# Kernel optimization log

Measured on AMD Instinct MI355X. Metric: run time of the kernel, lower is better.

The kernel has to match this reference:

```python
import jax, jax.numpy as jnp
import numpy as np

N, E, D, B = 40000, 100000, 64, 256

def setup_inputs() -> dict:
    key = jax.random.key(0)
    ks = jax.random.split(key, 32)
    p = lambda k, shp: jax.random.normal(k, shp, dtype=jnp.float32) * 0.1
    inp = {
        'n_feat': jax.random.normal(ks[0], (N, 23), dtype=jnp.float32),
        'e_feat': jax.random.normal(ks[1], (E, 19), dtype=jnp.float32),
        'src': jax.random.randint(ks[2], (E,), 0, N, dtype=jnp.int32),
        'dst': jax.random.randint(ks[3], (E,), 0, N, dtype=jnp.int32),
        'node_graph': jnp.sort(jax.random.randint(ks[4], (N,), 0, B, dtype=jnp.int32)),
        'batch_size': B,
        'lin0_w': p(ks[5], (D, 23)), 'lin0_b': p(ks[6], (D,)),
        'en_w1': p(ks[7], (128, 19)), 'en_b1': p(ks[8], (128,)),
        'en_w2': p(ks[9], (D * D, 128)), 'en_b2': p(ks[10], (D * D,)),
        'conv_b': p(ks[11], (D,)),
        'gru_wih': p(ks[12], (3 * D, D)), 'gru_whh': p(ks[13], (3 * D, D)),
        'gru_bih': p(ks[14], (3 * D,)), 'gru_bhh': p(ks[15], (3 * D,)),
        'ls_wih0': p(ks[16], (4 * D, 2 * D)), 'ls_wih12': p(ks[17], (2, 4 * D, D)),
        'ls_whh': p(ks[18], (3, 4 * D, D)),
        'ls_bih': p(ks[19], (3, 4 * D)), 'ls_bhh': p(ks[20], (3, 4 * D)),
        'lin3_w': p(ks[21], (2 * D, 2 * D)), 'lin3_b': p(ks[22], (2 * D,)),
        'pred_w': p(ks[23], (1, 2 * D)), 'pred_b': p(ks[24], (1,)),
    }
    return inp


def _gru_step(x, h, wih, whh, bih, bhh):
    gi = x @ wih.T + bih   # (N, 3D)
    gh = h @ whh.T + bhh
    i_r, i_z, i_n = jnp.split(gi, 3, axis=-1)
    h_r, h_z, h_n = jnp.split(gh, 3, axis=-1)
    r = jax.nn.sigmoid(i_r + h_r)
    z = jax.nn.sigmoid(i_z + h_z)
    n = jnp.tanh(i_n + r * h_n)
    return (1.0 - z) * n + z * h


def _lstm_cell(x, h, c, wih, whh, bih, bhh):
    g = x @ wih.T + bih + h @ whh.T + bhh  # (B, 4D)
    i, f, gg, o = jnp.split(g, 4, axis=-1)
    c2 = jax.nn.sigmoid(f) * c + jax.nn.sigmoid(i) * jnp.tanh(gg)
    h2 = jax.nn.sigmoid(o) * jnp.tanh(c2)
    return h2, c2


def reference(n_feat, e_feat, src, dst, node_graph, batch_size,
              lin0_w, lin0_b, en_w1, en_b1, en_w2, en_b2, conv_b,
              gru_wih, gru_whh, gru_bih, gru_bhh,
              ls_wih0, ls_wih12, ls_whh, ls_bih, ls_bhh,
              lin3_w, lin3_b, pred_w, pred_b):
    d = lin0_b.shape[0]
    n_nodes = n_feat.shape[0]
    # input projection
    out = n_feat @ lin0_w.T + lin0_b                       # (N, D)
    h = out                                                # GRU hidden (1 layer)
    # edge network (same every step) -> per-edge weight matrices
    ew = jax.nn.relu(e_feat @ en_w1.T + en_b1) @ en_w2.T + en_b2
    ew = ew.reshape(-1, d, d)                              # (E, D, D)
    for _ in range(6):
        msg = jnp.einsum('ed,edf->ef', out[src], ew)       # gather + per-edge GEMM
        m = jax.ops.segment_sum(msg, dst, num_segments=n_nodes) + conv_b
        h = _gru_step(m, h, gru_wih, gru_whh, gru_bih, gru_bhh)
        out = h
    # Set2Set pooling
    hs = [jnp.zeros((batch_size, d), jnp.float32) for _ in range(3)]
    cs = [jnp.zeros((batch_size, d), jnp.float32) for _ in range(3)]
    q_star = jnp.zeros((batch_size, 2 * d), jnp.float32)
    for _ in range(6):
        x = q_star
        for l in range(3):
            wih = ls_wih0 if l == 0 else ls_wih12[l - 1]
            hs[l], cs[l] = _lstm_cell(x, hs[l], cs[l], wih, ls_whh[l], ls_bih[l], ls_bhh[l])
            x = hs[l]
        q = x                                              # (B, D)
        e = jnp.sum(out * q[node_graph], axis=-1)          # (N,)
        emax = jax.ops.segment_max(e, node_graph, num_segments=batch_size)
        ee = jnp.exp(e - emax[node_graph])
        esum = jax.ops.segment_sum(ee, node_graph, num_segments=batch_size)
        alpha = (ee / esum[node_graph])[:, None]
        readout = jax.ops.segment_sum(out * alpha, node_graph, num_segments=batch_size)
        q_star = jnp.concatenate([q, readout], axis=-1)
    y = jax.nn.relu(q_star @ lin3_w.T + lin3_b)
    predict = y @ pred_w.T + pred_b
    return h[None], predict
```

## Files before the change

kernel.cpp:

```cpp
#include <hip/hip_runtime.h>

typedef unsigned short u16;
typedef unsigned int u32;
typedef _Float16 f16;
typedef __attribute__((ext_vector_type(8))) _Float16 f16x8;
typedef __attribute__((ext_vector_type(4))) _Float16 f16x4;
typedef __attribute__((ext_vector_type(4))) float f32x4;

#define NN 40000
#define EE 100000
#define DD 64
#define BB 256
#define XTS 136
#define EPB 128

__device__ inline float sigmoidf_(float x){
    return 1.f / (1.f + __expf(-x));
}
__device__ inline float tanhf_(float x){
    x = fmaxf(fminf(x, 15.f), -15.f);
    float e = __expf(2.f * x);
    return (e - 1.f) / (e + 1.f);
}

typedef __attribute__((address_space(3))) unsigned int lds_u32;
typedef __attribute__((address_space(1))) const unsigned int g_u32;
__device__ inline void gload_lds16(const void* g, void* l){
    __builtin_amdgcn_global_load_lds((g_u32*)g, (lds_u32*)l, 16, 0, 0);
}

__global__ __launch_bounds__(256) void prep_kernel(
    const float* __restrict__ en_w2, f16* __restrict__ w2h,
    const float* __restrict__ gru_wih, const float* __restrict__ gru_whh,
    f16* __restrict__ wf16h, f16* __restrict__ wf16l,
    const float* __restrict__ ls_wih0, const float* __restrict__ ls_wih12,
    const float* __restrict__ ls_whh, float* __restrict__ lsT,
    const float* __restrict__ lin3_w, float* __restrict__ lin3T,
    const float* __restrict__ gru_bih, const float* __restrict__ conv_b,
    float* __restrict__ effb,
    const int* __restrict__ node_graph, int* __restrict__ offs)
{
    int i = blockIdx.x * 256 + threadIdx.x;
    if (i < 524288){
        w2h[i] = (f16)en_w2[i];
        return;
    }
    i -= 524288;
    if (i < 49152){
        int sel = i / 12288;
        int r = i % 12288;
        int gg = sel >> 1, islo = sel & 1;
        float v = (gg ? gru_whh : gru_wih)[r];
        f16 hi = (f16)v;
        if (islo) wf16l[gg * 12288 + r] = (f16)(v - (float)hi);
        else      wf16h[gg * 12288 + r] = hi;
        return;
    }
    i -= 49152;
    if (i < 114688){
        float v;
        if (i < 32768){
            int d = i >> 8, g = i & 255;
            v = ls_wih0[g * 128 + d];
        } else if (i < 65536){
            int j = i - 32768;
            int l = j >> 14, r = j & 16383;
            int d = r >> 8, g = r & 255;
            v = ls_wih12[l * 16384 + g * 64 + d];
        } else {
            int j = i - 65536;
            int l = j >> 14, r = j & 16383;
            int d = r >> 8, g = r & 255;
            v = ls_whh[l * 16384 + g * 64 + d];
        }
        lsT[i] = v;
        return;
    }
    i -= 114688;
    if (i < 16384){
        int ii = i >> 7, jj = i & 127;
        lin3T[i] = lin3_w[jj * 128 + ii];
        return;
    }
    i -= 16384;
    if (i < 192){
        float b = gru_bih[i];
        #pragma unroll
        for (int d = 0; d < 64; d++) b += gru_wih[i * 64 + d] * conv_b[d];
        effb[i] = b;
        return;
    }
    i -= 192;
    if (i <= 256){
        int lo = 0, hi = NN;
        while (lo < hi){
            int mid = (lo + hi) >> 1;
            if (node_graph[mid] < i) lo = mid + 1; else hi = mid;
        }
        offs[i] = lo;
        return;
    }
}

__global__ __launch_bounds__(256) void lin0_kernel(
    const float* __restrict__ nf, const float* __restrict__ w,
    const float* __restrict__ b, float* __restrict__ out)
{
    int tid = blockIdx.x * 256 + threadIdx.x;
    int n = tid >> 6, d = tid & 63;
    if (n >= NN) return;
    float acc = b[d];
    const float* nr = nf + (size_t)n * 23;
    const float* wr = w + d * 23;
    #pragma unroll
    for (int j = 0; j < 23; j++) acc = fmaf(nr[j], wr[j], acc);
    out[(size_t)n * 64 + d] = acc;
}

__global__ __launch_bounds__(256) void edge_hidden_kernel(
    const float* __restrict__ ef, const float* __restrict__ w1,
    const float* __restrict__ b1, f16* __restrict__ hidh)
{
    int tid = blockIdx.x * 256 + threadIdx.x;
    int e = tid >> 7, k = tid & 127;
    if (e >= EE) return;
    float acc = b1[k];
    const float* er = ef + (size_t)e * 19;
    const float* wr = w1 + k * 19;
    #pragma unroll
    for (int j = 0; j < 19; j++) acc = fmaf(er[j], wr[j], acc);
    acc = fmaxf(acc, 0.f);
    hidh[(size_t)e * 128 + k] = (f16)acc;
}

__global__ __launch_bounds__(512) void msg_fused_kernel(
    const float* __restrict__ h, const f16* __restrict__ hidh,
    const f16* __restrict__ w2h, const float* __restrict__ b2,
    const int* __restrict__ src, const int* __restrict__ dst,
    float* __restrict__ m)
{
    __shared__ f16 s_xT[64 * XTS];
    __shared__ f16 s_b2f[4096];
    __shared__ int s_dst[EPB];
    __shared__ f16x8 s_t0[1024], s_t1[1024], s_t2[1024];

    const int t = threadIdx.x;
    const int base = blockIdx.x * EPB;
    const int lane = t & 63;
    const int wid = t >> 6;

    int goff[2], lbase[2];
    #pragma unroll
    for (int cc = 0; cc < 2; cc++){
        int s = cc * 512 + wid * 64 + lane;
        int kh = s >> 9;
        int c2 = s & 511;
        int col = c2 >> 3;
        int jj = (c2 & 7) ^ (col & 7);
        goff[cc] = col * 128 + kh * 64 + jj * 8;
        lbase[cc] = cc * 512 + wid * 64;
    }

#define STG_ISSUE(DN, BUF)                                                   \
    {                                                                        \
        const f16* gsrc = w2h + (size_t)(DN) * 8192;                         \
        gload_lds16(gsrc + goff[0], (BUF) + lbase[0]);                       \
        gload_lds16(gsrc + goff[1], (BUF) + lbase[1]);                       \
    }

    f16x8* pb0 = s_t0;
    f16x8* pb1 = s_t1;
    f16x8* pb2 = s_t2;
    STG_ISSUE(0, pb0);
    STG_ISSUE(1, pb1);

    for (int i = t; i < EPB * 64; i += 512){
        int el = i >> 6, f = i & 63;
        int e = base + el;
        float v = 0.f;
        if (e < EE) v = h[(size_t)src[e] * 64 + f];
        s_xT[f * XTS + el] = (f16)v;
    }
    for (int i = t; i < 4096; i += 512) s_b2f[i] = (f16)b2[i];
    if (t < EPB){
        int e = base + t;
        s_dst[t] = (e < EE) ? dst[e] : -1;
    }

    const int eg = wid >> 1;
    const int fp = wid & 1;
    const int r16 = lane & 15;
    const int kg = lane >> 4;
    const int we = eg * 32;
    const int sw = r16 & 7;

    f16x8 ah[2][4];
    #pragma unroll
    for (int mt = 0; mt < 2; mt++){
        int e = base + we + mt * 16 + r16;
        #pragma unroll
        for (int ks = 0; ks < 4; ks++){
            if (e < EE){
                ah[mt][ks] = *(const f16x8*)(hidh + (size_t)e * 128 + ks * 32 + kg * 8);
            } else {
                f16x8 z = {0,0,0,0,0,0,0,0};
                ah[mt][ks] = z;
            }
        }
    }

    f32x4 msg[2][2];
    #pragma unroll
    for (int a = 0; a < 2; a++)
        #pragma unroll
        for (int b = 0; b < 2; b++){
            f32x4 z = {0.f, 0.f, 0.f, 0.f};
            msg[a][b] = z;
        }

    int rslot[2][4];
    #pragma unroll
    for (int ftl = 0; ftl < 2; ftl++){
        int col = fp * 32 + ftl * 16 + r16;
        #pragma unroll
        for (int ks = 0; ks < 4; ks++){
            int j2 = (ks & 1) * 4 + kg;
            rslot[ftl][ks] = (ks >> 1) * 512 + col * 8 + (j2 ^ sw);
        }
    }

    __syncthreads();

    for (int d = 0; d < 64; d++){
        if (d + 2 < 64) STG_ISSUE(d + 2, pb2);
        f32x4 xv[2];
        #pragma unroll
        for (int mt = 0; mt < 2; mt++){
            f16x4 xh = *(const f16x4*)&s_xT[d * XTS + we + mt * 16 + kg * 4];
            #pragma unroll
            for (int r = 0; r < 4; r++) xv[mt][r] = (float)xh[r];
        }
        __builtin_amdgcn_s_setprio(1);
        #pragma unroll
        for (int ftl = 0; ftl < 2; ftl++){
            f16x8 bf0 = pb0[rslot[ftl][0]];
            f16x8 bf1 = pb0[rslot[ftl][1]];
            f16x8 bf2 = pb0[rslot[ftl][2]];
            f16x8 bf3 = pb0[rslot[ftl][3]];
            float b2v = (float)s_b2f[d * 64 + fp * 32 + ftl * 16 + r16];
            #pragma unroll
            for (int mt = 0; mt < 2; mt++){
                f32x4 acc = {b2v, b2v, b2v, b2v};
                acc = __builtin_amdgcn_mfma_f32_16x16x32_f16(ah[mt][0], bf0, acc, 0, 0, 0);
                acc = __builtin_amdgcn_mfma_f32_16x16x32_f16(ah[mt][1], bf1, acc, 0, 0, 0);
                acc = __builtin_amdgcn_mfma_f32_16x16x32_f16(ah[mt][2], bf2, acc, 0, 0, 0);
                acc = __builtin_amdgcn_mfma_f32_16x16x32_f16(ah[mt][3], bf3, acc, 0, 0, 0);
                msg[mt][ftl] = xv[mt] * acc + msg[mt][ftl];
            }
        }
        __builtin_amdgcn_s_setprio(0);
        if (d < 63){
            if (d <= 61) asm volatile("s_waitcnt vmcnt(2)" ::: "memory");
            else         asm volatile("s_waitcnt vmcnt(0)" ::: "memory");
            __builtin_amdgcn_s_barrier();
        }
        f16x8* tmp = pb0; pb0 = pb1; pb1 = pb2; pb2 = tmp;
    }
#undef STG_ISSUE

    #pragma unroll
    for (int mt = 0; mt < 2; mt++){
        #pragma unroll
        for (int r = 0; r < 4; r++){
            int el = we + mt * 16 + kg * 4 + r;
            int dt = s_dst[el];
            if (dt >= 0){
                #pragma unroll
                for (int ftl = 0; ftl < 2; ftl++)
                    atomicAdd(&m[(size_t)dt * 64 + fp * 32 + ftl * 16 + r16],
                              msg[mt][ftl][r]);
            }
        }
    }
}

__global__ __launch_bounds__(256) void gru_mfma_kernel(
    float* __restrict__ m, float* __restrict__ h,
    const f16* __restrict__ wf16h, const f16* __restrict__ wf16l,
    const float* __restrict__ effb, const float* __restrict__ bhh)
{
    __shared__ float s_g[2][32][194];
    const int t = threadIdx.x;
    const int base = blockIdx.x * 32;
    const int lane = t & 63;
    const int wid = t >> 6;
    const int rt = wid & 1;
    const int gg = wid >> 1;
    const int r16 = lane & 15;
    const int kg = lane >> 4;

    const float* __restrict__ X = gg ? h : m;
    int n = base + rt * 16 + r16;

    f16x8 ah[2], al[2];
    #pragma unroll
    for (int ks = 0; ks < 2; ks++){
        const float* xp = X + (size_t)n * 64 + ks * 32 + kg * 8;
        f32x4 v0 = *(const f32x4*)(xp);
        f32x4 v1 = *(const f32x4*)(xp + 4);
        #pragma unroll
        for (int j = 0; j < 4; j++){
            f16 hi0 = (f16)v0[j], hi1 = (f16)v1[j];
            ah[ks][j] = hi0;     ah[ks][4 + j] = hi1;
            al[ks][j] = (f16)(v0[j] - (float)hi0);
            al[ks][4 + j] = (f16)(v1[j] - (float)hi1);
        }
    }

    const f16* __restrict__ wh = wf16h + gg * 12288;
    const f16* __restrict__ wl = wf16l + gg * 12288;
    #pragma unroll
    for (int ct = 0; ct < 12; ct++){
        int g = ct * 16 + r16;
        f16x8 bh0 = *(const f16x8*)(wh + g * 64 + kg * 8);
        f16x8 bh1 = *(const f16x8*)(wh + g * 64 + 32 + kg * 8);
        f16x8 bl0 = *(const f16x8*)(wl + g * 64 + kg * 8);
        f16x8 bl1 = *(const f16x8*)(wl + g * 64 + 32 + kg * 8);
        f32x4 acc = {0.f, 0.f, 0.f, 0.f};
        acc = __builtin_amdgcn_mfma_f32_16x16x32_f16(ah[0], bh0, acc, 0, 0, 0);
        acc = __builtin_amdgcn_mfma_f32_16x16x32_f16(ah[1], bh1, acc, 0, 0, 0);
        acc = __builtin_amdgcn_mfma_f32_16x16x32_f16(ah[0], bl0, acc, 0, 0, 0);
        acc = __builtin_amdgcn_mfma_f32_16x16x32_f16(ah[1], bl1, acc, 0, 0, 0);
        acc = __builtin_amdgcn_mfma_f32_16x16x32_f16(al[0], bh0, acc, 0, 0, 0);
        acc = __builtin_amdgcn_mfma_f32_16x16x32_f16(al[1], bh1, acc, 0, 0, 0);
        #pragma unroll
        for (int r = 0; r < 4; r++)
            s_g[gg][rt * 16 + kg * 4 + r][ct * 16 + r16] = acc[r];
    }
    __syncthreads();

    int node = t >> 3;
    int f0 = (t & 7) * 8;
    int n2 = base + node;
    #pragma unroll
    for (int j = 0; j < 8; j++){
        int f = f0 + j;
        float gir = s_g[0][node][f]       + effb[f];
        float giz = s_g[0][node][64 + f]  + effb[64 + f];
        float gin = s_g[0][node][128 + f] + effb[128 + f];
        float ghr = s_g[1][node][f]       + bhh[f];
        float ghz = s_g[1][node][64 + f]  + bhh[64 + f];
        float ghn = s_g[1][node][128 + f] + bhh[128 + f];
        float r = sigmoidf_(gir + ghr);
        float z = sigmoidf_(giz + ghz);
        float nv = tanhf_(gin + r * ghn);
        size_t hb = (size_t)n2 * 64 + f;
        float hv = h[hb];
        h[hb] = (1.f - z) * nv + z * hv;
        m[hb] = 0.f;
    }
}

__global__ __launch_bounds__(256) void set2set_kernel(
    const float* __restrict__ out, const int* __restrict__ offs,
    const float* __restrict__ lsT, const float* __restrict__ ls_bih,
    const float* __restrict__ ls_bhh, const float* __restrict__ lin3T,
    const float* __restrict__ lin3_b, const float* __restrict__ pred_w,
    const float* __restrict__ pred_b, float* __restrict__ e_ws,
    float* __restrict__ pred_out)
{
    int g = blockIdx.x;
    int t = threadIdx.x;
    int ln = t >> 6, d = t & 63;
    __shared__ float s_qstar[128], s_h[3][64], s_c[3][64], s_g[256];
    __shared__ float s_r[4][64], s_red[4], s_wsum[4], s_y[128];
    if (t < 128) s_qstar[t] = 0.f;
    if (t < 192){ s_h[t / 64][t % 64] = 0.f; s_c[t / 64][t % 64] = 0.f; }
    int ns = offs[g], ne = offs[g + 1];
    __syncthreads();

#define LSTM_GATE(L)                                                         \
    __syncthreads();                                                         \
    s_g[t] = acc;                                                            \
    __syncthreads();                                                         \
    if (t < 64){                                                             \
        float iv = s_g[t], fv = s_g[64 + t], gv = s_g[128 + t], ov = s_g[192 + t]; \
        float c2 = sigmoidf_(fv) * s_c[L][t] + sigmoidf_(iv) * tanhf_(gv);   \
        float h2 = sigmoidf_(ov) * tanhf_(c2);                               \
        s_c[L][t] = c2; s_h[L][t] = h2;                                      \
    }                                                                        \
    __syncthreads();

    for (int it = 0; it < 6; it++){
        {
            float acc = ls_bih[t] + ls_bhh[t];
            const float* wx = lsT;
            #pragma unroll 32
            for (int j = 0; j < 128; j++) acc = fmaf(s_qstar[j], wx[j * 256 + t], acc);
            const float* wh = lsT + 65536;
            #pragma unroll 32
            for (int j = 0; j < 64; j++) acc = fmaf(s_h[0][j], wh[j * 256 + t], acc);
            LSTM_GATE(0)
        }
        {
            float acc = ls_bih[256 + t] + ls_bhh[256 + t];
            const float* wx = lsT + 32768;
            #pragma unroll 32
            for (int j = 0; j < 64; j++) acc = fmaf(s_h[0][j], wx[j * 256 + t], acc);
            const float* wh = lsT + 65536 + 16384;
            #pragma unroll 32
            for (int j = 0; j < 64; j++) acc = fmaf(s_h[1][j], wh[j * 256 + t], acc);
            LSTM_GATE(1)
        }
        {
            float acc = ls_bih[512 + t] + ls_bhh[512 + t];
            const float* wx = lsT + 32768 + 16384;
            #pragma unroll 32
            for (int j = 0; j < 64; j++) acc = fmaf(s_h[1][j], wx[j * 256 + t], acc);
            const float* wh = lsT + 65536 + 2 * 16384;
            #pragma unroll 32
            for (int j = 0; j < 64; j++) acc = fmaf(s_h[2][j], wh[j * 256 + t], acc);
            LSTM_GATE(2)
        }
        float wmax = -3.4e38f;
        #pragma unroll 2
        for (int n = ns + ln; n < ne; n += 4){
            float p = out[(size_t)n * 64 + d] * s_h[2][d];
            #pragma unroll
            for (int o = 1; o < 64; o <<= 1) p += __shfl_xor(p, o);
            if (d == 0) e_ws[n] = p;
            wmax = fmaxf(wmax, p);
        }
        if (d == 0) s_red[ln] = wmax;
        __syncthreads();
        float gmax = fmaxf(fmaxf(s_red[0], s_red[1]), fmaxf(s_red[2], s_red[3]));
        float wsum = 0.f, racc = 0.f;
        #pragma unroll 2
        for (int n = ns + ln; n < ne; n += 4){
            float w = __expf(e_ws[n] - gmax);
            wsum += w;
            racc = fmaf(w, out[(size_t)n * 64 + d], racc);
        }
        s_r[ln][d] = racc;
        if (d == 0) s_wsum[ln] = wsum;
        __syncthreads();
        if (t < 64){
            float gsum = s_wsum[0] + s_wsum[1] + s_wsum[2] + s_wsum[3];
            float ro = s_r[0][t] + s_r[1][t] + s_r[2][t] + s_r[3][t];
            ro = (gsum > 0.f) ? ro / gsum : 0.f;
            s_qstar[t] = s_h[2][t];
            s_qstar[64 + t] = ro;
        }
        __syncthreads();
    }
#undef LSTM_GATE
    if (t < 128){
        float acc = lin3_b[t];
        #pragma unroll 32
        for (int i = 0; i < 128; i++) acc = fmaf(s_qstar[i], lin3T[i * 128 + t], acc);
        s_y[t] = fmaxf(acc, 0.f);
    }
    __syncthreads();
    if (t < 64){
        float p = s_y[t] * pred_w[t] + s_y[64 + t] * pred_w[64 + t];
        #pragma unroll
        for (int o = 1; o < 64; o <<= 1) p += __shfl_xor(p, o);
        if (t == 0) pred_out[g] = p + pred_b[0];
    }
}

extern "C" void kernel_launch(void* const* d_in, const int* in_sizes, int n_in,
                              void* d_out, int out_size, void* d_ws, size_t ws_size,
                              hipStream_t stream)
{
    (void)in_sizes; (void)n_in; (void)out_size; (void)ws_size;
    const float* n_feat  = (const float*)d_in[0];
    const float* e_feat  = (const float*)d_in[1];
    const int*   src     = (const int*)d_in[2];
    const int*   dst     = (const int*)d_in[3];
    const int*   node_graph = (const int*)d_in[4];
    const float* lin0_w  = (const float*)d_in[6];
    const float* lin0_b  = (const float*)d_in[7];
    const float* en_w1   = (const float*)d_in[8];
    const float* en_b1   = (const float*)d_in[9];
    const float* en_w2   = (const float*)d_in[10];
    const float* en_b2   = (const float*)d_in[11];
    const float* conv_b  = (const float*)d_in[12];
    const float* gru_wih = (const float*)d_in[13];
    const float* gru_whh = (const float*)d_in[14];
    const float* gru_bih = (const float*)d_in[15];
    const float* gru_bhh = (const float*)d_in[16];
    const float* ls_wih0 = (const float*)d_in[17];
    const float* ls_wih12= (const float*)d_in[18];
    const float* ls_whh  = (const float*)d_in[19];
    const float* ls_bih  = (const float*)d_in[20];
    const float* ls_bhh  = (const float*)d_in[21];
    const float* lin3_w  = (const float*)d_in[22];
    const float* lin3_b  = (const float*)d_in[23];
    const float* pred_w  = (const float*)d_in[24];
    const float* pred_b  = (const float*)d_in[25];

    float* h = (float*)d_out;
    float* pred_out = (float*)d_out + (size_t)NN * 64;

    char* ws = (char*)d_ws;
    f16*   hidh  = (f16*)(ws + 0);
    float* m     = (float*)(ws + 25600000);
    f16*   w2h   = (f16*)(ws + 35840000);
    f16*   wf16h = (f16*)(ws + 36888576);
    f16*   wf16l = (f16*)(ws + 36937728);
    float* lsT   = (float*)(ws + 36986880);
    float* lin3T = (float*)(ws + 37445632);
    float* effb  = (float*)(ws + 37511168);
    float* e_ws  = (float*)(ws + 37511936);
    int*   offs  = (int*)(ws + 37671936);

    prep_kernel<<<2754, 256, 0, stream>>>(en_w2, w2h, gru_wih, gru_whh,
                                          wf16h, wf16l,
                                          ls_wih0, ls_wih12, ls_whh, lsT,
                                          lin3_w, lin3T, gru_bih, conv_b, effb,
                                          node_graph, offs);
    lin0_kernel<<<(NN * 64) / 256, 256, 0, stream>>>(n_feat, lin0_w, lin0_b, h);
    edge_hidden_kernel<<<(EE * 128) / 256, 256, 0, stream>>>(e_feat, en_w1, en_b1, hidh);
    hipMemsetAsync(m, 0, (size_t)NN * 64 * sizeof(float), stream);

    for (int step = 0; step < 6; step++){
        msg_fused_kernel<<<(EE + EPB - 1) / EPB, 512, 0, stream>>>(h, hidh, w2h,
                                                                   en_b2, src, dst, m);
        gru_mfma_kernel<<<NN / 32, 256, 0, stream>>>(m, h, wf16h, wf16l, effb, gru_bhh);
    }

    set2set_kernel<<<BB, 256, 0, stream>>>(h, offs, lsT, ls_bih, ls_bhh,
                                           lin3T, lin3_b, pred_w, pred_b,
                                           e_ws, pred_out);
}
```

Baseline: 1.269 ms.

## Use single-pass online softmax with vectorized loads in set2set attention

Replaces the two-pass attention in set2set (score pass writing scores to a workspace, then a max-normalised weighted sum) with a single-pass online softmax. Each 16-thread group handles one node per iteration using float4 loads, keeps a running max, sum and readout, and the 16 partial states are merged at the end. This avoids reading node features twice and the global score scratch buffer, at the cost of extra exp calls per node for rescaling. The set2set kernel is a small part of total time next to the message-passing loop.

Measured after the change: 1.180 ms, median of 2. 1.08x faster.

```diff
diff --git a/kernel.cpp b/kernel.cpp
--- a/kernel.cpp
+++ b/kernel.cpp
@@ -366,17 +366,18 @@
     const float* __restrict__ lsT, const float* __restrict__ ls_bih,
     const float* __restrict__ ls_bhh, const float* __restrict__ lin3T,
     const float* __restrict__ lin3_b, const float* __restrict__ pred_w,
-    const float* __restrict__ pred_b, float* __restrict__ e_ws,
-    float* __restrict__ pred_out)
+    const float* __restrict__ pred_b, float* __restrict__ pred_out)
 {
     int g = blockIdx.x;
     int t = threadIdx.x;
-    int ln = t >> 6, d = t & 63;
-    __shared__ float s_qstar[128], s_h[3][64], s_c[3][64], s_g[256];
-    __shared__ float s_r[4][64], s_red[4], s_wsum[4], s_y[128];
+    __shared__ float s_qstar[128], s_h[3][64], s_c[3][64], s_g[256], s_y[128];
+    __shared__ float s_gm[16], s_gw[16];
+    __shared__ float s_gr[16][68];
     if (t < 128) s_qstar[t] = 0.f;
     if (t < 192){ s_h[t / 64][t % 64] = 0.f; s_c[t / 64][t % 64] = 0.f; }
     int ns = offs[g], ne = offs[g + 1];
+    const int lg = t >> 4;
+    const int li = t & 15;
     __syncthreads();
 
 #define LSTM_GATE(L)                                                         \
@@ -422,31 +423,37 @@
             for (int j = 0; j < 64; j++) acc = fmaf(s_h[2][j], wh[j * 256 + t], acc);
             LSTM_GATE(2)
         }
-        float wmax = -3.4e38f;
-        #pragma unroll 2
-        for (int n = ns + ln; n < ne; n += 4){
-            float p = out[(size_t)n * 64 + d] * s_h[2][d];
-            #pragma unroll
-            for (int o = 1; o < 64; o <<= 1) p += __shfl_xor(p, o);
-            if (d == 0) e_ws[n] = p;
-            wmax = fmaxf(wmax, p);
-        }
-        if (d == 0) s_red[ln] = wmax;
-        __syncthreads();
-        float gmax = fmaxf(fmaxf(s_red[0], s_red[1]), fmaxf(s_red[2], s_red[3]));
-        float wsum = 0.f, racc = 0.f;
-        #pragma unroll 2
-        for (int n = ns + ln; n < ne; n += 4){
-            float w = __expf(e_ws[n] - gmax);
-            wsum += w;
-            racc = fmaf(w, out[(size_t)n * 64 + d], racc);
-        }
-        s_r[ln][d] = racc;
-        if (d == 0) s_wsum[ln] = wsum;
+        f32x4 qv = *(const f32x4*)&s_h[2][li * 4];
+        f32x4 racc = {0.f, 0.f, 0.f, 0.f};
+        float mrun = -3.4e38f, wsum = 0.f;
+        for (int n = ns + lg; n < ne; n += 16){
+            f32x4 ov = *(const f32x4*)&out[(size_t)n * 64 + li * 4];
+            float p = ov[0] * qv[0] + ov[1] * qv[1] + ov[2] * qv[2] + ov[3] * qv[3];
+            p += __shfl_xor(p, 1);
+            p += __shfl_xor(p, 2);
+            p += __shfl_xor(p, 4);
+            p += __shfl_xor(p, 8);
+            float mn = fmaxf(mrun, p);
+            float sc = __expf(mrun - mn);
+            float w = __expf(p - mn);
+            wsum = fmaf(wsum, sc, w);
+            racc = racc * sc + ov * w;
+            mrun = mn;
+        }
+        if (li == 0){ s_gm[lg] = mrun; s_gw[lg] = wsum; }
+        *(f32x4*)&s_gr[lg][li * 4] = racc;
         __syncthreads();
         if (t < 64){
-            float gsum = s_wsum[0] + s_wsum[1] + s_wsum[2] + s_wsum[3];
-            float ro = s_r[0][t] + s_r[1][t] + s_r[2][t] + s_r[3][t];
+            float gmax = -3.4e38f;
+            #pragma unroll
+            for (int g2 = 0; g2 < 16; g2++) gmax = fmaxf(gmax, s_gm[g2]);
+            float gsum = 0.f, ro = 0.f;
+            #pragma unroll
+            for (int g2 = 0; g2 < 16; g2++){
+                float e = __expf(s_gm[g2] - gmax);
+                gsum = fmaf(s_gw[g2], e, gsum);
+                ro = fmaf(s_gr[g2][t], e, ro);
+            }
             ro = (gsum > 0.f) ? ro / gsum : 0.f;
             s_qstar[t] = s_h[2][t];
             s_qstar[64 + t] = ro;
@@ -512,8 +519,7 @@
     float* lsT   = (float*)(ws + 36986880);
     float* lin3T = (float*)(ws + 37445632);
     float* effb  = (float*)(ws + 37511168);
-    float* e_ws  = (float*)(ws + 37511936);
-    int*   offs  = (int*)(ws + 37671936);
+    int*   offs  = (int*)(ws + 37511936);
 
     prep_kernel<<<2754, 256, 0, stream>>>(en_w2, w2h, gru_wih, gru_whh,
                                           wf16h, wf16l,
@@ -532,5 +538,5 @@
 
     set2set_kernel<<<BB, 256, 0, stream>>>(h, offs, lsT, ls_bih, ls_bhh,
                                            lin3T, lin3_b, pred_w, pred_b,
-                                           e_ws, pred_out);
-}
+                                           pred_out);
+}
```
